# Kernel tuning notes

Hardware: AMD Instinct MI355X
Metric: run time of the kernel (lower is better)

The kernel has to match this reference:

```python
import jax, jax.numpy as jnp
import numpy as np

N = 50000      # nodes
E = 800000     # edges (before self-loops)
IN = 256
HID = 256
OUT = 128
D = 4
K = 4
K1 = 8
NUM_KS = K1 * ((1 << K) - 1)   # 120 centroids
S = HID // D                   # sub-dim per quantization slice
TAU = 1.0


def setup_inputs() -> dict:
    key = jax.random.key(0)
    ks = jax.random.split(key, 9)
    x = jax.random.normal(ks[0], (N, IN), jnp.float32)
    edge_index = jax.random.randint(ks[1], (2, E), 0, N, dtype=jnp.int64)
    def lin(k, fan_in, fan_out):
        return jax.random.normal(k, (fan_in, fan_out), jnp.float32) / np.float32(np.sqrt(fan_in))
    W0 = lin(ks[2], IN, HID); b0 = jnp.zeros((HID,), jnp.float32)
    W1 = lin(ks[3], HID, HID); b1 = jnp.zeros((HID,), jnp.float32)
    W2 = lin(ks[4], HID, OUT); b2 = jnp.zeros((OUT,), jnp.float32)
    # kaiming_normal on (NUM_KS, HID): std = sqrt(2 / fan_in), fan_in = HID
    centroids = jax.random.normal(ks[5], (NUM_KS, HID), jnp.float32) * np.float32(np.sqrt(2.0 / HID))
    return dict(x=x, edge_index=edge_index, W0=W0, b0=b0, W1=W1, b1=b1, W2=W2, b2=b2,
                centroids=centroids)


def gcn_conv(x, W, b, src, dst):
    # PyG GCNConv: add self-loops, symmetric normalization, aggregate at target
    n = x.shape[0]
    loops = jnp.arange(n, dtype=src.dtype)
    s2 = jnp.concatenate([src, loops])
    d2 = jnp.concatenate([dst, loops])
    deg = jax.ops.segment_sum(jnp.ones_like(d2, x.dtype), d2, num_segments=n)
    dinv = jnp.where(deg > 0, jax.lax.rsqrt(deg), 0.0)
    norm = dinv[s2] * dinv[d2]                      # [E+n]
    xw = x @ W                                      # [n, out]
    out = jax.ops.segment_sum(xw[s2] * norm[:, None], d2, num_segments=n)
    return out + b


def quantize(H, C):
    # H: [n, HID], C: [NUM_KS, HID]
    n = H.shape[0]
    Hr = H.reshape(n, D, S)
    Cr = C.reshape(NUM_KS, D, S)
    # products[n,k,d] = sum_s H[n,d,s] * C[k,d,s]
    prods = jnp.einsum('nds,kds->nkd', Hr, Cr) / TAU   # [n, NUM_KS, D]
    soft_l, hard_l, prob_l = [], [], []
    off = 0
    d_idx = jnp.arange(D)[None, :]
    for j in range(K):                 # K fixed small groups of sizes k_1<<j
        m = K1 << j
        sl = prods[:, off:off + m, :]                  # [n, m, D]
        p = jax.nn.softmax(sl, axis=1)                 # scatter_softmax within group
        Cg = Cr[off:off + m]                           # [m, D, S]
        soft_l.append(jnp.einsum('nmd,mds->nds', p, Cg))
        idx = jnp.argmax(sl, axis=1)                   # [n, D] scatter_max within group
        hard_l.append(Cg[idx, d_idx, :])               # [n, D, S]
        prob_l.append(p)
        off += m
    soft = jnp.stack(soft_l, 1).reshape(n, K, HID)
    hard = jnp.stack(hard_l, 1).reshape(n, K, HID)
    q = jax.lax.stop_gradient(hard - soft) + soft      # straight-through
    balance = jnp.concatenate(prob_l, 1).sum(0) / n    # [NUM_KS, D]
    k_blns = jnp.concatenate([jnp.full((K1 << j,), 1.0 / (K1 << j), jnp.float32) for j in range(K)])
    target = jnp.broadcast_to(k_blns[:, None], (NUM_KS, D))
    reg = jnp.linalg.norm(balance - target)
    pred = jnp.max(q, axis=1)                          # [n, HID]
    return pred, reg


def reference(x, edge_index, W0, b0, W1, b1, W2, b2, centroids):
    src, dst = edge_index[0], edge_index[1]
    h = jax.nn.leaky_relu(gcn_conv(x, W0, b0, src, dst), negative_slope=0.5)
    h = jax.nn.leaky_relu(gcn_conv(h, W1, b1, src, dst), negative_slope=0.5)
    pred, reg = quantize(h, centroids)
    h = h + pred
    out = gcn_conv(h, W2, b2, src, dst)
    return out, reg
```

## Files before the change

### kernel.cpp

```cpp
#include <hip/hip_runtime.h>
#include <math.h>


typedef short bf16x8 __attribute__((ext_vector_type(8)));
typedef float f32x4 __attribute__((ext_vector_type(4)));

__device__ __forceinline__ unsigned short bf16_rne(float a) {
    unsigned u = __builtin_bit_cast(unsigned, a);
    return (unsigned short)((u + 0x7FFFu + ((u >> 16) & 1u)) >> 16);
}
__device__ __forceinline__ float bf16_to_f(unsigned short h) {
    return __builtin_bit_cast(float, (unsigned)h << 16);
}
__device__ __forceinline__ void split4(const float* e, unsigned short* h, unsigned short* l) {
#pragma unroll
    for (int t = 0; t < 4; ++t) {
        h[t] = bf16_rne(e[t]);
        l[t] = bf16_rne(e[t] - bf16_to_f(h[t]));
    }
}


__global__ void k_init(int* cnt, int* cursor, int* counter, float* balance, int n) {
    int i = blockIdx.x * blockDim.x + threadIdx.x;
    if (i < n) { cnt[i] = 0; cursor[i] = 0; }
    if (i < 480) balance[i] = 0.f;
    if (i == 0) *counter = 0;
}

__global__ void k_count(const int* __restrict__ dst, int* __restrict__ cnt, int e) {
    int i = blockIdx.x * blockDim.x + threadIdx.x;
    if (i < e) atomicAdd(&cnt[dst[i]], 1);
}

__global__ void k_dinv(const int* __restrict__ cnt, float* __restrict__ dinv, int n) {
    int i = blockIdx.x * blockDim.x + threadIdx.x;
    if (i < n) dinv[i] = rsqrtf((float)cnt[i] + 1.0f);
}

__global__ void k_alloc(const int* __restrict__ cnt, int* __restrict__ row_start,
                        int* __restrict__ counter, int n) {
    int i = blockIdx.x * blockDim.x + threadIdx.x;
    if (i < n) row_start[i] = atomicAdd(counter, cnt[i]);
}

__global__ void k_fill(const int* __restrict__ src, const int* __restrict__ dst,
                       const float* __restrict__ dinv, const int* __restrict__ row_start,
                       int* __restrict__ cursor, int* __restrict__ csr_src,
                       float* __restrict__ csr_norm, int e) {
    int i = blockIdx.x * blockDim.x + threadIdx.x;
    if (i >= e) return;
    int s = src[i], d = dst[i];
    int slot = atomicAdd(&cursor[d], 1);
    int idx = row_start[d] + slot;
    csr_src[idx] = s;
    csr_norm[idx] = dinv[s] * dinv[d];
}


__global__ void k_splitW(const float* __restrict__ W, short* __restrict__ Th,
                         short* __restrict__ Tl, int N) {
    int i = blockIdx.x * blockDim.x + threadIdx.x;
    if (i >= N * 256) return;
    int nn = i >> 8, kk = i & 255;
    float v = W[kk * N + nn];
    unsigned short h = bf16_rne(v);
    unsigned short l = bf16_rne(v - bf16_to_f(h));
    Th[i] = (short)h;
    Tl[i] = (short)l;
}

__global__ void k_splitA(const float* __restrict__ X, short* __restrict__ Hi,
                         short* __restrict__ Lo, int total8) {
    int i = blockIdx.x * blockDim.x + threadIdx.x;
    if (i >= total8) return;
    float4 a = *(const float4*)(X + (size_t)i * 8);
    float4 b = *(const float4*)(X + (size_t)i * 8 + 4);
    float e0[4] = {a.x, a.y, a.z, a.w}, e1[4] = {b.x, b.y, b.z, b.w};
    unsigned short h0[4], l0[4], h1[4], l1[4];
    split4(e0, h0, l0);
    split4(e1, h1, l1);
    *(uint4*)(Hi + (size_t)i * 8) = make_uint4(h0[0] | (h0[1] << 16), h0[2] | (h0[3] << 16),
                                              h1[0] | (h1[1] << 16), h1[2] | (h1[3] << 16));
    *(uint4*)(Lo + (size_t)i * 8) = make_uint4(l0[0] | (l0[1] << 16), l0[2] | (l0[3] << 16),
                                              l1[0] | (l1[1] << 16), l1[2] | (l1[3] << 16));
}


__global__ __launch_bounds__(256, 2) void k_gemm_bf16s(const short* __restrict__ Ah,
                                                       const short* __restrict__ Al,
                                                       const short* __restrict__ Bh,
                                                       const short* __restrict__ Bl,
                                                       float* __restrict__ C,
                                                       int M, int N) {
    __shared__ short smem[4 * 128 * 56];
    short* Ash = smem;
    short* Asl = smem + 7168;
    short* Bsh = smem + 14336;
    short* Bsl = smem + 21504;
    const int tid = threadIdx.x;
    const int bm = blockIdx.x * 128;
    const int bn = blockIdx.y * 128;
    const int wave = tid >> 6, lane = tid & 63;
    const int wr = wave >> 1, wc = wave & 1;
    const int lr = lane & 15, lk = lane >> 4;

    int srow[2], ssg[2];
    bool aval[2];
#pragma unroll
    for (int it = 0; it < 2; ++it) {
        int u = it * 256 + tid;
        srow[it] = u >> 2;
        ssg[it] = (u & 3) << 3;
        aval[it] = (bm + srow[it]) < M;
    }

    const bf16x8 z8 = {0, 0, 0, 0, 0, 0, 0, 0};
    bf16x8 pah[2], pal[2], pbh[2], pbl[2];

    auto prefetch = [&](int k0) {
#pragma unroll
        for (int it = 0; it < 2; ++it) {
            size_t arow = (size_t)(bm + srow[it]) * 256 + k0 + ssg[it];
            size_t brow = (size_t)(bn + srow[it]) * 256 + k0 + ssg[it];
            pah[it] = aval[it] ? *(const bf16x8*)(Ah + arow) : z8;
            pal[it] = aval[it] ? *(const bf16x8*)(Al + arow) : z8;
            pbh[it] = *(const bf16x8*)(Bh + brow);
            pbl[it] = *(const bf16x8*)(Bl + brow);
        }
    };

    f32x4 acc[4][4] = {};
    prefetch(0);

    for (int k0 = 0; k0 < 256; k0 += 32) {
#pragma unroll
        for (int it = 0; it < 2; ++it) {
            int off = srow[it] * 56 + ssg[it];
            *(bf16x8*)&Ash[off] = pah[it];
            *(bf16x8*)&Asl[off] = pal[it];
            *(bf16x8*)&Bsh[off] = pbh[it];
            *(bf16x8*)&Bsl[off] = pbl[it];
        }
        __syncthreads();

        bf16x8 ah[4], al[4], bh[4], bl[4];
#pragma unroll
        for (int i = 0; i < 4; ++i) {
            int off = (wr * 64 + i * 16 + lr) * 56 + lk * 8;
            ah[i] = *(bf16x8*)&Ash[off];
            al[i] = *(bf16x8*)&Asl[off];
        }
#pragma unroll
        for (int j = 0; j < 4; ++j) {
            int off = (wc * 64 + j * 16 + lr) * 56 + lk * 8;
            bh[j] = *(bf16x8*)&Bsh[off];
            bl[j] = *(bf16x8*)&Bsl[off];
        }

        if (k0 < 224) prefetch(k0 + 32);

#pragma unroll
        for (int i = 0; i < 4; ++i)
#pragma unroll
            for (int j = 0; j < 4; ++j) {
                acc[i][j] = __builtin_amdgcn_mfma_f32_16x16x32_bf16(al[i], bh[j], acc[i][j], 0, 0, 0);
                acc[i][j] = __builtin_amdgcn_mfma_f32_16x16x32_bf16(ah[i], bl[j], acc[i][j], 0, 0, 0);
                acc[i][j] = __builtin_amdgcn_mfma_f32_16x16x32_bf16(ah[i], bh[j], acc[i][j], 0, 0, 0);
            }
        __syncthreads();
    }

    float* Cs = (float*)smem;
#pragma unroll
    for (int p = 0; p < 2; ++p) {
        if (wc == p) {
#pragma unroll
            for (int i = 0; i < 4; ++i)
#pragma unroll
                for (int r = 0; r < 4; ++r) {
                    int row = wr * 64 + i * 16 + lk * 4 + r;
#pragma unroll
                    for (int j = 0; j < 4; ++j)
                        Cs[row * 68 + j * 16 + lr] = acc[i][j][r];
                }
        }
        __syncthreads();
#pragma unroll
        for (int t = 0; t < 8; ++t) {
            int idx = t * 256 + tid;
            int row = idx >> 4, c4 = idx & 15;
            if (bm + row < M)
                *(float4*)(C + (size_t)(bm + row) * N + bn + p * 64 + c4 * 4) =
                    *(const float4*)&Cs[row * 68 + c4 * 4];
        }
        __syncthreads();
    }
}


template <bool RELU, int MODE>
__global__ __launch_bounds__(256, 4) void k_agg4(const float* __restrict__ xw,
                                                 const float* __restrict__ dinv,
                                                 const int* __restrict__ csr_src,
                                                 const float* __restrict__ csr_norm,
                                                 const int* __restrict__ row_start,
                                                 const int* __restrict__ cnt,
                                                 const float* __restrict__ bias,
                                                 float* __restrict__ out,
                                                 short* __restrict__ outH,
                                                 short* __restrict__ outL, int n) {
    int node = blockIdx.x * 4 + (threadIdx.x >> 6);
    if (node >= n) return;
    int lane = threadIdx.x & 63;
    int c = lane * 4;
    float di = dinv[node];
    float4 self = *(const float4*)(xw + (size_t)node * 256 + c);
    float4 bv = *(const float4*)(bias + c);
    float sw = di * di;
    float ax = self.x * sw + bv.x;
    float ay = self.y * sw + bv.y;
    float az = self.z * sw + bv.z;
    float aw = self.w * sw + bv.w;
    int st = row_start[node];
    int m = cnt[node];
    for (int t0 = 0; t0 < m; t0 += 64) {
        int rem = m - t0;
        int cnt_i = rem < 64 ? rem : 64;
        int idx_l = 0;
        float nrm_l = 0.f;
        if (lane < cnt_i) {
            idx_l = csr_src[st + t0 + lane];
            nrm_l = csr_norm[st + t0 + lane];
        }
        int t = 0;
        for (; t + 8 <= cnt_i; t += 8) {
            const float* p0 = xw + (size_t)__shfl(idx_l, t + 0, 64) * 256 + c;
            const float* p1 = xw + (size_t)__shfl(idx_l, t + 1, 64) * 256 + c;
            const float* p2 = xw + (size_t)__shfl(idx_l, t + 2, 64) * 256 + c;
            const float* p3 = xw + (size_t)__shfl(idx_l, t + 3, 64) * 256 + c;
            const float* p4 = xw + (size_t)__shfl(idx_l, t + 4, 64) * 256 + c;
            const float* p5 = xw + (size_t)__shfl(idx_l, t + 5, 64) * 256 + c;
            const float* p6 = xw + (size_t)__shfl(idx_l, t + 6, 64) * 256 + c;
            const float* p7 = xw + (size_t)__shfl(idx_l, t + 7, 64) * 256 + c;
            float4 v0 = *(const float4*)p0;
            float4 v1 = *(const float4*)p1;
            float4 v2 = *(const float4*)p2;
            float4 v3 = *(const float4*)p3;
            float4 v4 = *(const float4*)p4;
            float4 v5 = *(const float4*)p5;
            float4 v6 = *(const float4*)p6;
            float4 v7 = *(const float4*)p7;
            float w0 = __shfl(nrm_l, t + 0, 64);
            float w1 = __shfl(nrm_l, t + 1, 64);
            float w2 = __shfl(nrm_l, t + 2, 64);
            float w3 = __shfl(nrm_l, t + 3, 64);
            float w4 = __shfl(nrm_l, t + 4, 64);
            float w5 = __shfl(nrm_l, t + 5, 64);
            float w6 = __shfl(nrm_l, t + 6, 64);
            float w7 = __shfl(nrm_l, t + 7, 64);
            ax += v0.x * w0; ay += v0.y * w0; az += v0.z * w0; aw += v0.w * w0;
            ax += v1.x * w1; ay += v1.y * w1; az += v1.z * w1; aw += v1.w * w1;
            ax += v2.x * w2; ay += v2.y * w2; az += v2.z * w2; aw += v2.w * w2;
            ax += v3.x * w3; ay += v3.y * w3; az += v3.z * w3; aw += v3.w * w3;
            ax += v4.x * w4; ay += v4.y * w4; az += v4.z * w4; aw += v4.w * w4;
            ax += v5.x * w5; ay += v5.y * w5; az += v5.z * w5; aw += v5.w * w5;
            ax += v6.x * w6; ay += v6.y * w6; az += v6.z * w6; aw += v6.w * w6;
            ax += v7.x * w7; ay += v7.y * w7; az += v7.z * w7; aw += v7.w * w7;
        }
        for (; t < cnt_i; ++t) {
            int s = __shfl(idx_l, t, 64);
            float w = __shfl(nrm_l, t, 64);
            float4 v = *(const float4*)(xw + (size_t)s * 256 + c);
            ax += v.x * w; ay += v.y * w; az += v.z * w; aw += v.w * w;
        }
    }
    if (RELU) {
        ax = ax > 0.f ? ax : 0.5f * ax;
        ay = ay > 0.f ? ay : 0.5f * ay;
        az = az > 0.f ? az : 0.5f * az;
        aw = aw > 0.f ? aw : 0.5f * aw;
    }
    if (MODE == 0) {
        *(float4*)(out + (size_t)node * 256 + c) = make_float4(ax, ay, az, aw);
    } else {
        float e[4] = {ax, ay, az, aw};
        unsigned short h[4], l[4];
        split4(e, h, l);
        size_t o = (size_t)node * 256 + c;
        *(uint2*)(outH + o) = make_uint2(h[0] | (h[1] << 16), h[2] | (h[3] << 16));
        *(uint2*)(outL + o) = make_uint2(l[0] | (l[1] << 16), l[2] | (l[3] << 16));
    }
}

__global__ __launch_bounds__(256, 4) void k_agg2(const float* __restrict__ xw,
                                                 const float* __restrict__ dinv,
                                                 const int* __restrict__ csr_src,
                                                 const float* __restrict__ csr_norm,
                                                 const int* __restrict__ row_start,
                                                 const int* __restrict__ cnt,
                                                 const float* __restrict__ bias,
                                                 float* __restrict__ out, int n) {
    int node = blockIdx.x * 4 + (threadIdx.x >> 6);
    if (node >= n) return;
    int lane = threadIdx.x & 63;
    int c = lane * 2;
    float di = dinv[node];
    float2 self = *(const float2*)(xw + (size_t)node * 128 + c);
    float2 bv = *(const float2*)(bias + c);
    float sw = di * di;
    float ax = self.x * sw + bv.x;
    float ay = self.y * sw + bv.y;
    int st = row_start[node];
    int m = cnt[node];
    for (int t0 = 0; t0 < m; t0 += 64) {
        int rem = m - t0;
        int cnt_i = rem < 64 ? rem : 64;
        int idx_l = 0;
        float nrm_l = 0.f;
        if (lane < cnt_i) {
            idx_l = csr_src[st + t0 + lane];
            nrm_l = csr_norm[st + t0 + lane];
        }
        int t = 0;
        for (; t + 8 <= cnt_i; t += 8) {
            const float* p0 = xw + (size_t)__shfl(idx_l, t + 0, 64) * 128 + c;
            const float* p1 = xw + (size_t)__shfl(idx_l, t + 1, 64) * 128 + c;
            const float* p2 = xw + (size_t)__shfl(idx_l, t + 2, 64) * 128 + c;
            const float* p3 = xw + (size_t)__shfl(idx_l, t + 3, 64) * 128 + c;
            const float* p4 = xw + (size_t)__shfl(idx_l, t + 4, 64) * 128 + c;
            const float* p5 = xw + (size_t)__shfl(idx_l, t + 5, 64) * 128 + c;
            const float* p6 = xw + (size_t)__shfl(idx_l, t + 6, 64) * 128 + c;
            const float* p7 = xw + (size_t)__shfl(idx_l, t + 7, 64) * 128 + c;
            float2 v0 = *(const float2*)p0;
            float2 v1 = *(const float2*)p1;
            float2 v2 = *(const float2*)p2;
            float2 v3 = *(const float2*)p3;
            float2 v4 = *(const float2*)p4;
            float2 v5 = *(const float2*)p5;
            float2 v6 = *(const float2*)p6;
            float2 v7 = *(const float2*)p7;
            float w0 = __shfl(nrm_l, t + 0, 64);
            float w1 = __shfl(nrm_l, t + 1, 64);
            float w2 = __shfl(nrm_l, t + 2, 64);
            float w3 = __shfl(nrm_l, t + 3, 64);
            float w4 = __shfl(nrm_l, t + 4, 64);
            float w5 = __shfl(nrm_l, t + 5, 64);
            float w6 = __shfl(nrm_l, t + 6, 64);
            float w7 = __shfl(nrm_l, t + 7, 64);
            ax += v0.x * w0; ay += v0.y * w0;
            ax += v1.x * w1; ay += v1.y * w1;
            ax += v2.x * w2; ay += v2.y * w2;
            ax += v3.x * w3; ay += v3.y * w3;
            ax += v4.x * w4; ay += v4.y * w4;
            ax += v5.x * w5; ay += v5.y * w5;
            ax += v6.x * w6; ay += v6.y * w6;
            ax += v7.x * w7; ay += v7.y * w7;
        }
        for (; t < cnt_i; ++t) {
            int s = __shfl(idx_l, t, 64);
            float w = __shfl(nrm_l, t, 64);
            float2 v = *(const float2*)(xw + (size_t)s * 128 + c);
            ax += v.x * w; ay += v.y * w;
        }
    }
    *(float2*)(out + (size_t)node * 128 + c) = make_float2(ax, ay);
}


__global__ __launch_bounds__(256, 4) void k_quant4(const float* __restrict__ h2,
                                                   const float* __restrict__ cent,
                                                   short* __restrict__ h3h,
                                                   short* __restrict__ h3l,
                                                   float* __restrict__ balance_g, int n) {
    __shared__ float As[32 * 132];
    __shared__ float Bs[32 * 132];
    __shared__ float bal4[4 * 128];
    __shared__ int km_ls[128 * 4];
    const int tid = threadIdx.x;
    const int n0 = blockIdx.x * 128;
    const int d = blockIdx.y;
    const int ty = tid >> 4, tx = tid & 15;
    const int wave = tid >> 6, lane = tid & 63;

    int gid, base, sz;
    if (tx == 0)       { gid = 0; base = 0;  sz = 1; }
    else if (tx <= 2)  { gid = 1; base = 1;  sz = 2; }
    else if (tx <= 6)  { gid = 2; base = 3;  sz = 4; }
    else if (tx <= 14) { gid = 3; base = 7;  sz = 8; }
    else               { gid = 0; base = 15; sz = 0; }
    const int l = tx - base;
    const int segbase = lane & 48;

    {
        int k = tid >> 3, r = tid & 7;
        int col = (r < 4) ? (60 + r) : (120 + r);
        Bs[k * 132 + col] = 0.f;
    }

    const int srow = tid >> 3, sk4 = tid & 7;
    const bool srv = (n0 + srow) < n;
    float acc[8][8] = {};

#pragma unroll
    for (int it = 0; it < 4; ++it) {
        int row = srow + it * 32;
        float4 v = make_float4(0.f, 0.f, 0.f, 0.f);
        if (n0 + row < n)
            v = *(const float4*)(h2 + (size_t)(n0 + row) * 256 + d * 64 + sk4 * 4);
        As[(sk4 * 4 + 0) * 132 + row] = v.x;
        As[(sk4 * 4 + 1) * 132 + row] = v.y;
        As[(sk4 * 4 + 2) * 132 + row] = v.z;
        As[(sk4 * 4 + 3) * 132 + row] = v.w;
    }
#pragma unroll
    for (int it = 0; it < 4; ++it) {
        int q = it * 256 + tid;
        if (q < 960) {
            int cc = q >> 3, k4 = q & 7;
            float4 v = *(const float4*)(cent + (size_t)cc * 256 + d * 64 + k4 * 4);
            int col = ((cc >> 3) << 2) + (((cc >> 2) & 1) << 6) + (cc & 3);
            Bs[(k4 * 4 + 0) * 132 + col] = v.x;
            Bs[(k4 * 4 + 1) * 132 + col] = v.y;
            Bs[(k4 * 4 + 2) * 132 + col] = v.z;
            Bs[(k4 * 4 + 3) * 132 + col] = v.w;
        }
    }
    float4 ph[4];
#pragma unroll
    for (int it = 0; it < 4; ++it) {
        int row = srow + it * 32;
        ph[it] = make_float4(0.f, 0.f, 0.f, 0.f);
        if (n0 + row < n)
            ph[it] = *(const float4*)(h2 + (size_t)(n0 + row) * 256 + d * 64 + 32 + sk4 * 4);
    }
    __syncthreads();

#pragma unroll 4
    for (int k = 0; k < 32; ++k) {
        float4 a0 = *(const float4*)&As[k * 132 + ty * 8];
        float4 a1 = *(const float4*)&As[k * 132 + ty * 8 + 4];
        float4 b0 = *(const float4*)&Bs[k * 132 + tx * 4];
        float4 b1 = *(const float4*)&Bs[k * 132 + 64 + tx * 4];
        float av[8] = {a0.x, a0.y, a0.z, a0.w, a1.x, a1.y, a1.z, a1.w};
        float bv[8] = {b0.x, b0.y, b0.z, b0.w, b1.x, b1.y, b1.z, b1.w};
#pragma unroll
        for (int i = 0; i < 8; ++i)
#pragma unroll
            for (int j = 0; j < 8; ++j)
                acc[i][j] += av[i] * bv[j];
    }
    __syncthreads();

#pragma unroll
    for (int it = 0; it < 4; ++it) {
        int row = srow + it * 32;
        As[(sk4 * 4 + 0) * 132 + row] = ph[it].x;
        As[(sk4 * 4 + 1) * 132 + row] = ph[it].y;
        As[(sk4 * 4 + 2) * 132 + row] = ph[it].z;
        As[(sk4 * 4 + 3) * 132 + row] = ph[it].w;
    }
#pragma unroll
    for (int it = 0; it < 4; ++it) {
        int q = it * 256 + tid;
        if (q < 960) {
            int cc = q >> 3, k4 = q & 7;
            float4 v = *(const float4*)(cent + (size_t)cc * 256 + d * 64 + 32 + k4 * 4);
            int col = ((cc >> 3) << 2) + (((cc >> 2) & 1) << 6) + (cc & 3);
            Bs[(k4 * 4 + 0) * 132 + col] = v.x;
            Bs[(k4 * 4 + 1) * 132 + col] = v.y;
            Bs[(k4 * 4 + 2) * 132 + col] = v.z;
            Bs[(k4 * 4 + 3) * 132 + col] = v.w;
        }
    }
    __syncthreads();

#pragma unroll 4
    for (int k = 0; k < 32; ++k) {
        float4 a0 = *(const float4*)&As[k * 132 + ty * 8];
        float4 a1 = *(const float4*)&As[k * 132 + ty * 8 + 4];
        float4 b0 = *(const float4*)&Bs[k * 132 + tx * 4];
        float4 b1 = *(const float4*)&Bs[k * 132 + 64 + tx * 4];
        float av[8] = {a0.x, a0.y, a0.z, a0.w, a1.x, a1.y, a1.z, a1.w};
        float bv[8] = {b0.x, b0.y, b0.z, b0.w, b1.x, b1.y, b1.z, b1.w};
#pragma unroll
        for (int i = 0; i < 8; ++i)
#pragma unroll
            for (int j = 0; j < 8; ++j)
                acc[i][j] += av[i] * bv[j];
    }

    float balp[8] = {};
#pragma unroll
    for (int i = 0; i < 8; ++i) {
        const int node = ty * 8 + i;
        const bool act = (n0 + node) < n;
        float m = acc[i][0];
        int am = tx * 8;
#pragma unroll
        for (int j = 1; j < 8; ++j)
            if (acc[i][j] > m) { m = acc[i][j]; am = tx * 8 + j; }
#pragma unroll
        for (int s = 1; s <= 4; s <<= 1) {
            int pl = l ^ s;
            int srcl = segbase + base + pl;
            float mo = __shfl(m, srcl, 64);
            int amo = __shfl(am, srcl, 64);
            if (pl < sz && (mo > m || (mo == m && amo < am))) { m = mo; am = amo; }
        }
        float Z = 0.f;
#pragma unroll
        for (int j = 0; j < 8; ++j) {
            float e2 = expf(acc[i][j] - m);
            acc[i][j] = e2;
            Z += e2;
        }
#pragma unroll
        for (int s = 1; s <= 4; s <<= 1) {
            int pl = l ^ s;
            int srcl = segbase + base + pl;
            float Zo = __shfl(Z, srcl, 64);
            if (pl < sz) Z += Zo;
        }
        float invZ = (act && sz > 0) ? (1.0f / Z) : 0.f;
#pragma unroll
        for (int j = 0; j < 8; ++j) balp[j] += acc[i][j] * invZ;
        if (l == 0 && sz > 0) km_ls[node * 4 + gid] = am;
    }

#pragma unroll
    for (int j = 0; j < 8; ++j) {
        float v = balp[j];
        v += __shfl_xor(v, 16, 64);
        v += __shfl_xor(v, 32, 64);
        balp[j] = v;
    }
    if (lane < 16) {
#pragma unroll
        for (int j = 0; j < 8; ++j)
            bal4[wave * 128 + tx * 8 + j] = balp[j];
    }
    __syncthreads();
    if (tid < 120) {
        float s = bal4[tid] + bal4[128 + tid] + bal4[256 + tid] + bal4[384 + tid];
        atomicAdd(&balance_g[tid * 4 + d], s);
    }

    {
        const int node = tid >> 1;
        const int half = tid & 1;
        if (n0 + node < n) {
            int k0 = km_ls[node * 4 + 0], k1 = km_ls[node * 4 + 1];
            int k2 = km_ls[node * 4 + 2], k3 = km_ls[node * 4 + 3];
            const float* hp = h2 + (size_t)(n0 + node) * 256 + d * 64 + half * 32;
            const float* c0 = cent + (size_t)k0 * 256 + d * 64 + half * 32;
            const float* c1 = cent + (size_t)k1 * 256 + d * 64 + half * 32;
            const float* c2 = cent + (size_t)k2 * 256 + d * 64 + half * 32;
            const float* c3 = cent + (size_t)k3 * 256 + d * 64 + half * 32;
            size_t obase = (size_t)(n0 + node) * 256 + d * 64 + half * 32;
#pragma unroll
            for (int q = 0; q < 8; ++q) {
                int g = q * 4;
                float4 hv = *(const float4*)(hp + g);
                float4 v0 = *(const float4*)(c0 + g);
                float4 v1 = *(const float4*)(c1 + g);
                float4 v2 = *(const float4*)(c2 + g);
                float4 v3 = *(const float4*)(c3 + g);
                float e[4];
                e[0] = hv.x + fmaxf(fmaxf(v0.x, v1.x), fmaxf(v2.x, v3.x));
                e[1] = hv.y + fmaxf(fmaxf(v0.y, v1.y), fmaxf(v2.y, v3.y));
                e[2] = hv.z + fmaxf(fmaxf(v0.z, v1.z), fmaxf(v2.z, v3.z));
                e[3] = hv.w + fmaxf(fmaxf(v0.w, v1.w), fmaxf(v2.w, v3.w));
                unsigned short h[4], l[4];
                split4(e, h, l);
                *(uint2*)(h3h + obase + g) = make_uint2(h[0] | (h[1] << 16), h[2] | (h[3] << 16));
                *(uint2*)(h3l + obase + g) = make_uint2(l[0] | (l[1] << 16), l[2] | (l[3] << 16));
            }
        }
    }
}

__global__ void k_reg(const float* __restrict__ balance_g, float* __restrict__ out_reg,
                      float inv_n) {
    __shared__ float red[512];
    int tid = threadIdx.x;
    float v = 0.f;
    if (tid < 480) {
        int k = tid >> 2;
        float target = (k < 8) ? 0.125f : (k < 24) ? 0.0625f : (k < 56) ? 0.03125f : 0.015625f;
        float b = balance_g[tid] * inv_n;
        float df = b - target;
        v = df * df;
    }
    red[tid] = v;
    __syncthreads();
    for (int s = 256; s > 0; s >>= 1) {
        if (tid < s) red[tid] += red[tid + s];
        __syncthreads();
    }
    if (tid == 0) *out_reg = sqrtf(red[0]);
}


extern "C" void kernel_launch(void* const* d_in, const int* in_sizes, int n_in,
                              void* d_out, int out_size, void* d_ws, size_t ws_size,
                              hipStream_t stream) {
    const float* x    = (const float*)d_in[0];
    const int*   ei   = (const int*)d_in[1];
    const float* W0   = (const float*)d_in[2];
    const float* b0   = (const float*)d_in[3];
    const float* W1   = (const float*)d_in[4];
    const float* b1   = (const float*)d_in[5];
    const float* W2   = (const float*)d_in[6];
    const float* b2   = (const float*)d_in[7];
    const float* cent = (const float*)d_in[8];
    const int n = in_sizes[0] / 256;
    const int e = in_sizes[1] / 2;
    const int* src = ei;
    const int* dst = ei + e;
    float* out = (float*)d_out;

    char* w = (char*)d_ws;
    float* bufA = (float*)w;      w += (size_t)n * 256 * 4;
    float* bufB = (float*)w;      w += (size_t)n * 256 * 4;
    float* dinv = (float*)w;      w += (size_t)n * 4;
    int* cnt = (int*)w;           w += (size_t)n * 4;
    int* row_start = (int*)w;     w += (size_t)n * 4;
    int* cursor = (int*)w;        w += (size_t)n * 4;
    int* csr_src = (int*)w;       w += (size_t)e * 4;
    float* csr_norm = (float*)w;  w += (size_t)e * 4;
    int* counter = (int*)w;       w += 256;
    float* balance = (float*)w;   w += 480 * 4;
    short* w0h = (short*)w;       w += 256 * 256 * 2;
    short* w0l = (short*)w;       w += 256 * 256 * 2;
    short* w1h = (short*)w;       w += 256 * 256 * 2;
    short* w1l = (short*)w;       w += 256 * 256 * 2;
    short* w2h = (short*)w;       w += 128 * 256 * 2;
    short* w2l = (short*)w;       w += 128 * 256 * 2;

    short* xh = (short*)bufA;
    short* xl = xh + (size_t)n * 256;
    short* h1h = (short*)bufA;
    short* h1l = h1h + (size_t)n * 256;
    short* h3h = (short*)bufB;
    short* h3l = h3h + (size_t)n * 256;

    const int tb = 256;
    k_init<<<(n + tb - 1) / tb, tb, 0, stream>>>(cnt, cursor, counter, balance, n);
    k_count<<<(e + tb - 1) / tb, tb, 0, stream>>>(dst, cnt, e);
    k_dinv<<<(n + tb - 1) / tb, tb, 0, stream>>>(cnt, dinv, n);
    k_alloc<<<(n + tb - 1) / tb, tb, 0, stream>>>(cnt, row_start, counter, n);
    k_fill<<<(e + tb - 1) / tb, tb, 0, stream>>>(src, dst, dinv, row_start, cursor,
                                                 csr_src, csr_norm, e);

    k_splitW<<<(256 * 256 + tb - 1) / tb, tb, 0, stream>>>(W0, w0h, w0l, 256);
    k_splitW<<<(256 * 256 + tb - 1) / tb, tb, 0, stream>>>(W1, w1h, w1l, 256);
    k_splitW<<<(128 * 256 + tb - 1) / tb, tb, 0, stream>>>(W2, w2h, w2l, 128);
    k_splitA<<<(n * 32 + tb - 1) / tb, tb, 0, stream>>>(x, xh, xl, n * 32);

    dim3 g1((n + 127) / 128, 2);
    k_gemm_bf16s<<<g1, 256, 0, stream>>>(xh, xl, w0h, w0l, bufB, n, 256);
    k_agg4<true, 1><<<(n + 3) / 4, 256, 0, stream>>>(bufB, dinv, csr_src, csr_norm,
                                                     row_start, cnt, b0, nullptr,
                                                     h1h, h1l, n);
    k_gemm_bf16s<<<g1, 256, 0, stream>>>(h1h, h1l, w1h, w1l, bufB, n, 256);
    k_agg4<true, 0><<<(n + 3) / 4, 256, 0, stream>>>(bufB, dinv, csr_src, csr_norm,
                                                     row_start, cnt, b1, bufA,
                                                     nullptr, nullptr, n);

    dim3 gq((n + 127) / 128, 4);
    k_quant4<<<gq, 256, 0, stream>>>(bufA, cent, h3h, h3l, balance, n);

    dim3 g3((n + 127) / 128, 1);
    k_gemm_bf16s<<<g3, 256, 0, stream>>>(h3h, h3l, w2h, w2l, bufA, n, 128);
    k_agg2<<<(n + 3) / 4, 256, 0, stream>>>(bufA, dinv, csr_src, csr_norm,
                                            row_start, cnt, b2, out, n);
    k_reg<<<1, 512, 0, stream>>>(balance, out + (size_t)n * 128, 1.0f / (float)n);
}
```

Baseline: 611.7 us.

## Fold GCN normalization into GEMM epilogue and move quantizer to split-bf16 MFMA

Result: slower. 652.0 us (+6.6%).

```diff
diff --git a/kernel.cpp b/kernel.cpp
--- a/kernel.cpp
+++ b/kernel.cpp
@@ -33,41 +33,49 @@
     if (i < e) atomicAdd(&cnt[dst[i]], 1);
 }
 
-__global__ void k_dinv(const int* __restrict__ cnt, float* __restrict__ dinv, int n) {
+__global__ void k_allocdinv(const int* __restrict__ cnt, int* __restrict__ row_start,
+                            int* __restrict__ counter, float* __restrict__ dinv, int n) {
     int i = blockIdx.x * blockDim.x + threadIdx.x;
-    if (i < n) dinv[i] = rsqrtf((float)cnt[i] + 1.0f);
-}
-
-__global__ void k_alloc(const int* __restrict__ cnt, int* __restrict__ row_start,
-                        int* __restrict__ counter, int n) {
-    int i = blockIdx.x * blockDim.x + threadIdx.x;
-    if (i < n) row_start[i] = atomicAdd(counter, cnt[i]);
+    if (i < n) {
+        row_start[i] = atomicAdd(counter, cnt[i]);
+        dinv[i] = rsqrtf((float)cnt[i] + 1.0f);
+    }
 }
 
 __global__ void k_fill(const int* __restrict__ src, const int* __restrict__ dst,
-                       const float* __restrict__ dinv, const int* __restrict__ row_start,
-                       int* __restrict__ cursor, int* __restrict__ csr_src,
-                       float* __restrict__ csr_norm, int e) {
+                       const int* __restrict__ row_start, int* __restrict__ cursor,
+                       int* __restrict__ csr_src, int e) {
     int i = blockIdx.x * blockDim.x + threadIdx.x;
     if (i >= e) return;
     int s = src[i], d = dst[i];
     int slot = atomicAdd(&cursor[d], 1);
-    int idx = row_start[d] + slot;
-    csr_src[idx] = s;
-    csr_norm[idx] = dinv[s] * dinv[d];
-}
-
-
-__global__ void k_splitW(const float* __restrict__ W, short* __restrict__ Th,
-                         short* __restrict__ Tl, int N) {
+    csr_src[row_start[d] + slot] = s;
+}
+
+
+__global__ void k_splitWC(const float* __restrict__ W0, const float* __restrict__ W1,
+                          const float* __restrict__ W2, const float* __restrict__ cent,
+                          short* __restrict__ w0h, short* __restrict__ w0l,
+                          short* __restrict__ w1h, short* __restrict__ w1l,
+                          short* __restrict__ w2h, short* __restrict__ w2l,
+                          short* __restrict__ ch, short* __restrict__ cl) {
     int i = blockIdx.x * blockDim.x + threadIdx.x;
-    if (i >= N * 256) return;
-    int nn = i >> 8, kk = i & 255;
-    float v = W[kk * N + nn];
+    float v;
+    short *ph, *pl;
+    int j;
+    if (i < 65536) {
+        j = i; v = W0[(j & 255) * 256 + (j >> 8)]; ph = w0h; pl = w0l;
+    } else if (i < 131072) {
+        j = i - 65536; v = W1[(j & 255) * 256 + (j >> 8)]; ph = w1h; pl = w1l;
+    } else if (i < 163840) {
+        j = i - 131072; v = W2[(j & 255) * 128 + (j >> 8)]; ph = w2h; pl = w2l;
+    } else {
+        j = i - 163840; int c = j >> 8;
+        v = (c < 120) ? cent[j] : 0.f; ph = ch; pl = cl;
+    }
     unsigned short h = bf16_rne(v);
-    unsigned short l = bf16_rne(v - bf16_to_f(h));
-    Th[i] = (short)h;
-    Tl[i] = (short)l;
+    ph[j] = (short)h;
+    pl[j] = (short)bf16_rne(v - bf16_to_f(h));
 }
 
 __global__ void k_splitA(const float* __restrict__ X, short* __restrict__ Hi,
@@ -91,6 +99,7 @@
                                                        const short* __restrict__ Al,
                                                        const short* __restrict__ Bh,
                                                        const short* __restrict__ Bl,
+                                                       const float* __restrict__ dinv,
                                                        float* __restrict__ C,
                                                        int M, int N) {
     __shared__ short smem[4 * 128 * 56];
@@ -190,9 +199,12 @@
         for (int t = 0; t < 8; ++t) {
             int idx = t * 256 + tid;
             int row = idx >> 4, c4 = idx & 15;
-            if (bm + row < M)
-                *(float4*)(C + (size_t)(bm + row) * N + bn + p * 64 + c4 * 4) =
-                    *(const float4*)&Cs[row * 68 + c4 * 4];
+            if (bm + row < M) {
+                float s = dinv[bm + row];
+                float4 v = *(const float4*)&Cs[row * 68 + c4 * 4];
+                v.x *= s; v.y *= s; v.z *= s; v.w *= s;
+                *(float4*)(C + (size_t)(bm + row) * N + bn + p * 64 + c4 * 4) = v;
+            }
         }
         __syncthreads();
     }
@@ -203,7 +215,6 @@
 __global__ __launch_bounds__(256, 4) void k_agg4(const float* __restrict__ xw,
                                                  const float* __restrict__ dinv,
                                                  const int* __restrict__ csr_src,
-                                                 const float* __restrict__ csr_norm,
                                                  const int* __restrict__ row_start,
                                                  const int* __restrict__ cnt,
                                                  const float* __restrict__ bias,
@@ -214,25 +225,15 @@
     if (node >= n) return;
     int lane = threadIdx.x & 63;
     int c = lane * 4;
-    float di = dinv[node];
     float4 self = *(const float4*)(xw + (size_t)node * 256 + c);
-    float4 bv = *(const float4*)(bias + c);
-    float sw = di * di;
-    float ax = self.x * sw + bv.x;
-    float ay = self.y * sw + bv.y;
-    float az = self.z * sw + bv.z;
-    float aw = self.w * sw + bv.w;
+    float ax = self.x, ay = self.y, az = self.z, aw = self.w;
     int st = row_start[node];
     int m = cnt[node];
     for (int t0 = 0; t0 < m; t0 += 64) {
         int rem = m - t0;
         int cnt_i = rem < 64 ? rem : 64;
         int idx_l = 0;
-        float nrm_l = 0.f;
-        if (lane < cnt_i) {
-            idx_l = csr_src[st + t0 + lane];
-            nrm_l = csr_norm[st + t0 + lane];
-        }
+        if (lane < cnt_i) idx_l = csr_src[st + t0 + lane];
         int t = 0;
         for (; t + 8 <= cnt_i; t += 8) {
             const float* p0 = xw + (size_t)__shfl(idx_l, t + 0, 64) * 256 + c;
@@ -251,30 +252,27 @@
             float4 v5 = *(const float4*)p5;
             float4 v6 = *(const float4*)p6;
             float4 v7 = *(const float4*)p7;
-            float w0 = __shfl(nrm_l, t + 0, 64);
-            float w1 = __shfl(nrm_l, t + 1, 64);
-            float w2 = __shfl(nrm_l, t + 2, 64);
-            float w3 = __shfl(nrm_l, t + 3, 64);
-            float w4 = __shfl(nrm_l, t + 4, 64);
-            float w5 = __shfl(nrm_l, t + 5, 64);
-            float w6 = __shfl(nrm_l, t + 6, 64);
-            float w7 = __shfl(nrm_l, t + 7, 64);
-            ax += v0.x * w0; ay += v0.y * w0; az += v0.z * w0; aw += v0.w * w0;
-            ax += v1.x * w1; ay += v1.y * w1; az += v1.z * w1; aw += v1.w * w1;
-            ax += v2.x * w2; ay += v2.y * w2; az += v2.z * w2; aw += v2.w * w2;
-            ax += v3.x * w3; ay += v3.y * w3; az += v3.z * w3; aw += v3.w * w3;
-            ax += v4.x * w4; ay += v4.y * w4; az += v4.z * w4; aw += v4.w * w4;
-            ax += v5.x * w5; ay += v5.y * w5; az += v5.z * w5; aw += v5.w * w5;
-            ax += v6.x * w6; ay += v6.y * w6; az += v6.z * w6; aw += v6.w * w6;
-            ax += v7.x * w7; ay += v7.y * w7; az += v7.z * w7; aw += v7.w * w7;
+            ax += v0.x; ay += v0.y; az += v0.z; aw += v0.w;
+            ax += v1.x; ay += v1.y; az += v1.z; aw += v1.w;
+            ax += v2.x; ay += v2.y; az += v2.z; aw += v2.w;
+            ax += v3.x; ay += v3.y; az += v3.z; aw += v3.w;
+            ax += v4.x; ay += v4.y; az += v4.z; aw += v4.w;
+            ax += v5.x; ay += v5.y; az += v5.z; aw += v5.w;
+            ax += v6.x; ay += v6.y; az += v6.z; aw += v6.w;
+            ax += v7.x; ay += v7.y; az += v7.z; aw += v7.w;
         }
         for (; t < cnt_i; ++t) {
             int s = __shfl(idx_l, t, 64);
-            float w = __shfl(nrm_l, t, 64);
             float4 v = *(const float4*)(xw + (size_t)s * 256 + c);
-            ax += v.x * w; ay += v.y * w; az += v.z * w; aw += v.w * w;
-        }
-    }
+            ax += v.x; ay += v.y; az += v.z; aw += v.w;
+        }
+    }
+    float di = dinv[node];
+    float4 bv = *(const float4*)(bias + c);
+    ax = ax * di + bv.x;
+    ay = ay * di + bv.y;
+    az = az * di + bv.z;
+    aw = aw * di + bv.w;
     if (RELU) {
         ax = ax > 0.f ? ax : 0.5f * ax;
         ay = ay > 0.f ? ay : 0.5f * ay;
@@ -296,7 +294,6 @@
 __global__ __launch_bounds__(256, 4) void k_agg2(const float* __restrict__ xw,
                                                  const float* __restrict__ dinv,
                                                  const int* __restrict__ csr_src,
-                                                 const float* __restrict__ csr_norm,
                                                  const int* __restrict__ row_start,
                                                  const int* __restrict__ cnt,
                                                  const float* __restrict__ bias,
@@ -305,23 +302,15 @@
     if (node >= n) return;
     int lane = threadIdx.x & 63;
     int c = lane * 2;
-    float di = dinv[node];
     float2 self = *(const float2*)(xw + (size_t)node * 128 + c);
-    float2 bv = *(const float2*)(bias + c);
-    float sw = di * di;
-    float ax = self.x * sw + bv.x;
-    float ay = self.y * sw + bv.y;
+    float ax = self.x, ay = self.y;
     int st = row_start[node];
     int m = cnt[node];
     for (int t0 = 0; t0 < m; t0 += 64) {
         int rem = m - t0;
         int cnt_i = rem < 64 ? rem : 64;
         int idx_l = 0;
-        float nrm_l = 0.f;
-        if (lane < cnt_i) {
-            idx_l = csr_src[st + t0 + lane];
-            nrm_l = csr_norm[st + t0 + lane];
-        }
+        if (lane < cnt_i) idx_l = csr_src[st + t0 + lane];
         int t = 0;
         for (; t + 8 <= cnt_i; t += 8) {
             const float* p0 = xw + (size_t)__shfl(idx_l, t + 0, 64) * 128 + c;
@@ -340,205 +329,167 @@
             float2 v5 = *(const float2*)p5;
             float2 v6 = *(const float2*)p6;
             float2 v7 = *(const float2*)p7;
-            float w0 = __shfl(nrm_l, t + 0, 64);
-            float w1 = __shfl(nrm_l, t + 1, 64);
-            float w2 = __shfl(nrm_l, t + 2, 64);
-            float w3 = __shfl(nrm_l, t + 3, 64);
-            float w4 = __shfl(nrm_l, t + 4, 64);
-            float w5 = __shfl(nrm_l, t + 5, 64);
-            float w6 = __shfl(nrm_l, t + 6, 64);
-            float w7 = __shfl(nrm_l, t + 7, 64);
-            ax += v0.x * w0; ay += v0.y * w0;
-            ax += v1.x * w1; ay += v1.y * w1;
-            ax += v2.x * w2; ay += v2.y * w2;
-            ax += v3.x * w3; ay += v3.y * w3;
-            ax += v4.x * w4; ay += v4.y * w4;
-            ax += v5.x * w5; ay += v5.y * w5;
-            ax += v6.x * w6; ay += v6.y * w6;
-            ax += v7.x * w7; ay += v7.y * w7;
+            ax += v0.x; ay += v0.y;
+            ax += v1.x; ay += v1.y;
+            ax += v2.x; ay += v2.y;
+            ax += v3.x; ay += v3.y;
+            ax += v4.x; ay += v4.y;
+            ax += v5.x; ay += v5.y;
+            ax += v6.x; ay += v6.y;
+            ax += v7.x; ay += v7.y;
         }
         for (; t < cnt_i; ++t) {
             int s = __shfl(idx_l, t, 64);
-            float w = __shfl(nrm_l, t, 64);
             float2 v = *(const float2*)(xw + (size_t)s * 128 + c);
-            ax += v.x * w; ay += v.y * w;
-        }
-    }
-    *(float2*)(out + (size_t)node * 128 + c) = make_float2(ax, ay);
-}
-
-
-__global__ __launch_bounds__(256, 4) void k_quant4(const float* __restrict__ h2,
+            ax += v.x; ay += v.y;
+        }
+    }
+    float di = dinv[node];
+    float2 bv = *(const float2*)(bias + c);
+    *(float2*)(out + (size_t)node * 128 + c) = make_float2(ax * di + bv.x, ay * di + bv.y);
+}
+
+
+__global__ __launch_bounds__(256, 3) void k_quant6(const short* __restrict__ h2h,
+                                                   const short* __restrict__ h2l,
+                                                   const short* __restrict__ ch,
+                                                   const short* __restrict__ cl,
                                                    const float* __restrict__ cent,
                                                    short* __restrict__ h3h,
                                                    short* __restrict__ h3l,
                                                    float* __restrict__ balance_g, int n) {
-    __shared__ float As[32 * 132];
-    __shared__ float Bs[32 * 132];
+    __shared__ short Ah[128 * 72];
+    __shared__ short Al[128 * 72];
     __shared__ float bal4[4 * 128];
     __shared__ int km_ls[128 * 4];
     const int tid = threadIdx.x;
     const int n0 = blockIdx.x * 128;
     const int d = blockIdx.y;
-    const int ty = tid >> 4, tx = tid & 15;
     const int wave = tid >> 6, lane = tid & 63;
-
-    int gid, base, sz;
-    if (tx == 0)       { gid = 0; base = 0;  sz = 1; }
-    else if (tx <= 2)  { gid = 1; base = 1;  sz = 2; }
-    else if (tx <= 6)  { gid = 2; base = 3;  sz = 4; }
-    else if (tx <= 14) { gid = 3; base = 7;  sz = 8; }
-    else               { gid = 0; base = 15; sz = 0; }
-    const int l = tx - base;
-    const int segbase = lane & 48;
+    const int l = lane & 15, lk = lane >> 4;
+    const int nib = lane & 48;
 
     {
-        int k = tid >> 3, r = tid & 7;
-        int col = (r < 4) ? (60 + r) : (120 + r);
-        Bs[k * 132 + col] = 0.f;
-    }
-
-    const int srow = tid >> 3, sk4 = tid & 7;
-    const bool srv = (n0 + srow) < n;
-    float acc[8][8] = {};
-
-#pragma unroll
-    for (int it = 0; it < 4; ++it) {
-        int row = srow + it * 32;
-        float4 v = make_float4(0.f, 0.f, 0.f, 0.f);
-        if (n0 + row < n)
-            v = *(const float4*)(h2 + (size_t)(n0 + row) * 256 + d * 64 + sk4 * 4);
-        As[(sk4 * 4 + 0) * 132 + row] = v.x;
-        As[(sk4 * 4 + 1) * 132 + row] = v.y;
-        As[(sk4 * 4 + 2) * 132 + row] = v.z;
-        As[(sk4 * 4 + 3) * 132 + row] = v.w;
-    }
-#pragma unroll
-    for (int it = 0; it < 4; ++it) {
-        int q = it * 256 + tid;
-        if (q < 960) {
-            int cc = q >> 3, k4 = q & 7;
-            float4 v = *(const float4*)(cent + (size_t)cc * 256 + d * 64 + k4 * 4);
-            int col = ((cc >> 3) << 2) + (((cc >> 2) & 1) << 6) + (cc & 3);
-            Bs[(k4 * 4 + 0) * 132 + col] = v.x;
-            Bs[(k4 * 4 + 1) * 132 + col] = v.y;
-            Bs[(k4 * 4 + 2) * 132 + col] = v.z;
-            Bs[(k4 * 4 + 3) * 132 + col] = v.w;
-        }
-    }
-    float4 ph[4];
-#pragma unroll
-    for (int it = 0; it < 4; ++it) {
-        int row = srow + it * 32;
-        ph[it] = make_float4(0.f, 0.f, 0.f, 0.f);
-        if (n0 + row < n)
-            ph[it] = *(const float4*)(h2 + (size_t)(n0 + row) * 256 + d * 64 + 32 + sk4 * 4);
+        const int row = tid >> 1, half = tid & 1;
+        const size_t g = (size_t)(n0 + row) * 256 + d * 64 + half * 32;
+        const int o = row * 72 + half * 32;
+        const bf16x8 z8 = {0, 0, 0, 0, 0, 0, 0, 0};
+        bool v = (n0 + row) < n;
+#pragma unroll
+        for (int s = 0; s < 4; ++s) {
+            *(bf16x8*)&Ah[o + s * 8] = v ? *(const bf16x8*)(h2h + g + s * 8) : z8;
+            *(bf16x8*)&Al[o + s * 8] = v ? *(const bf16x8*)(h2l + g + s * 8) : z8;
+        }
     }
     __syncthreads();
 
-#pragma unroll 4
-    for (int k = 0; k < 32; ++k) {
-        float4 a0 = *(const float4*)&As[k * 132 + ty * 8];
-        float4 a1 = *(const float4*)&As[k * 132 + ty * 8 + 4];
-        float4 b0 = *(const float4*)&Bs[k * 132 + tx * 4];
-        float4 b1 = *(const float4*)&Bs[k * 132 + 64 + tx * 4];
-        float av[8] = {a0.x, a0.y, a0.z, a0.w, a1.x, a1.y, a1.z, a1.w};
-        float bv[8] = {b0.x, b0.y, b0.z, b0.w, b1.x, b1.y, b1.z, b1.w};
-#pragma unroll
-        for (int i = 0; i < 8; ++i)
-#pragma unroll
-            for (int j = 0; j < 8; ++j)
-                acc[i][j] += av[i] * bv[j];
-    }
-    __syncthreads();
-
-#pragma unroll
-    for (int it = 0; it < 4; ++it) {
-        int row = srow + it * 32;
-        As[(sk4 * 4 + 0) * 132 + row] = ph[it].x;
-        As[(sk4 * 4 + 1) * 132 + row] = ph[it].y;
-        As[(sk4 * 4 + 2) * 132 + row] = ph[it].z;
-        As[(sk4 * 4 + 3) * 132 + row] = ph[it].w;
-    }
-#pragma unroll
-    for (int it = 0; it < 4; ++it) {
-        int q = it * 256 + tid;
-        if (q < 960) {
-            int cc = q >> 3, k4 = q & 7;
-            float4 v = *(const float4*)(cent + (size_t)cc * 256 + d * 64 + 32 + k4 * 4);
-            int col = ((cc >> 3) << 2) + (((cc >> 2) & 1) << 6) + (cc & 3);
-            Bs[(k4 * 4 + 0) * 132 + col] = v.x;
-            Bs[(k4 * 4 + 1) * 132 + col] = v.y;
-            Bs[(k4 * 4 + 2) * 132 + col] = v.z;
-            Bs[(k4 * 4 + 3) * 132 + col] = v.w;
-        }
-    }
-    __syncthreads();
-
-#pragma unroll 4
-    for (int k = 0; k < 32; ++k) {
-        float4 a0 = *(const float4*)&As[k * 132 + ty * 8];
-        float4 a1 = *(const float4*)&As[k * 132 + ty * 8 + 4];
-        float4 b0 = *(const float4*)&Bs[k * 132 + tx * 4];
-        float4 b1 = *(const float4*)&Bs[k * 132 + 64 + tx * 4];
-        float av[8] = {a0.x, a0.y, a0.z, a0.w, a1.x, a1.y, a1.z, a1.w};
-        float bv[8] = {b0.x, b0.y, b0.z, b0.w, b1.x, b1.y, b1.z, b1.w};
-#pragma unroll
-        for (int i = 0; i < 8; ++i)
-#pragma unroll
-            for (int j = 0; j < 8; ++j)
-                acc[i][j] += av[i] * bv[j];
-    }
+    f32x4 acc[2][8] = {};
+#pragma unroll
+    for (int kc = 0; kc < 2; ++kc) {
+        bf16x8 ah[2], al[2];
+#pragma unroll
+        for (int t = 0; t < 2; ++t) {
+            int off = (wave * 32 + t * 16 + l) * 72 + kc * 32 + lk * 8;
+            ah[t] = *(const bf16x8*)&Ah[off];
+            al[t] = *(const bf16x8*)&Al[off];
+        }
+#pragma unroll
+        for (int ct = 0; ct < 8; ++ct) {
+            size_t boff = (size_t)(ct * 16 + l) * 256 + d * 64 + kc * 32 + lk * 8;
+            bf16x8 bh = *(const bf16x8*)(ch + boff);
+            bf16x8 bl = *(const bf16x8*)(cl + boff);
+#pragma unroll
+            for (int t = 0; t < 2; ++t) {
+                acc[t][ct] = __builtin_amdgcn_mfma_f32_16x16x32_bf16(al[t], bh, acc[t][ct], 0, 0, 0);
+                acc[t][ct] = __builtin_amdgcn_mfma_f32_16x16x32_bf16(ah[t], bl, acc[t][ct], 0, 0, 0);
+                acc[t][ct] = __builtin_amdgcn_mfma_f32_16x16x32_bf16(ah[t], bh, acc[t][ct], 0, 0, 0);
+            }
+        }
+    }
+
+    int gof[8];
+    gof[0] = (l < 8) ? 0 : 1;
+    gof[1] = (l < 8) ? 1 : 2;
+    gof[2] = 2;
+    gof[3] = (l < 8) ? 2 : 3;
+    gof[4] = 3; gof[5] = 3; gof[6] = 3;
+    gof[7] = (l < 8) ? 3 : -1;
 
     float balp[8] = {};
-#pragma unroll
-    for (int i = 0; i < 8; ++i) {
-        const int node = ty * 8 + i;
-        const bool act = (n0 + node) < n;
-        float m = acc[i][0];
-        int am = tx * 8;
-#pragma unroll
-        for (int j = 1; j < 8; ++j)
-            if (acc[i][j] > m) { m = acc[i][j]; am = tx * 8 + j; }
-#pragma unroll
-        for (int s = 1; s <= 4; s <<= 1) {
-            int pl = l ^ s;
-            int srcl = segbase + base + pl;
-            float mo = __shfl(m, srcl, 64);
-            int amo = __shfl(am, srcl, 64);
-            if (pl < sz && (mo > m || (mo == m && amo < am))) { m = mo; am = amo; }
-        }
-        float Z = 0.f;
-#pragma unroll
-        for (int j = 0; j < 8; ++j) {
-            float e2 = expf(acc[i][j] - m);
-            acc[i][j] = e2;
-            Z += e2;
-        }
-#pragma unroll
-        for (int s = 1; s <= 4; s <<= 1) {
-            int pl = l ^ s;
-            int srcl = segbase + base + pl;
-            float Zo = __shfl(Z, srcl, 64);
-            if (pl < sz) Z += Zo;
-        }
-        float invZ = (act && sz > 0) ? (1.0f / Z) : 0.f;
-#pragma unroll
-        for (int j = 0; j < 8; ++j) balp[j] += acc[i][j] * invZ;
-        if (l == 0 && sz > 0) km_ls[node * 4 + gid] = am;
-    }
-
-#pragma unroll
-    for (int j = 0; j < 8; ++j) {
-        float v = balp[j];
-        v += __shfl_xor(v, 16, 64);
-        v += __shfl_xor(v, 32, 64);
-        balp[j] = v;
+
+#pragma unroll
+    for (int t = 0; t < 2; ++t)
+#pragma unroll
+        for (int r = 0; r < 4; ++r) {
+            const int node = wave * 32 + t * 16 + lk * 4 + r;
+            const bool act = (n0 + node) < n;
+            float v[8];
+#pragma unroll
+            for (int ct = 0; ct < 8; ++ct) v[ct] = acc[t][ct][r];
+
+            float mg[4];
+            int ag[4];
+#pragma unroll
+            for (int g = 0; g < 4; ++g) {
+                float m = -3.4e38f;
+                int am = 0x7FFFFFFF;
+#pragma unroll
+                for (int ct = 0; ct < 8; ++ct)
+                    if (gof[ct] == g && v[ct] > m) { m = v[ct]; am = ct * 16 + l; }
+#pragma unroll
+                for (int s = 1; s <= 8; s <<= 1) {
+                    int srcl = nib | (l ^ s);
+                    float mo = __shfl(m, srcl, 64);
+                    int amo = __shfl(am, srcl, 64);
+                    if (mo > m || (mo == m && amo < am)) { m = mo; am = amo; }
+                }
+                mg[g] = m;
+                ag[g] = am;
+            }
+            float e[8];
+            float Z[4] = {0.f, 0.f, 0.f, 0.f};
+#pragma unroll
+            for (int ct = 0; ct < 8; ++ct) {
+                float ms = (gof[ct] == 0) ? mg[0] : (gof[ct] == 1) ? mg[1]
+                         : (gof[ct] == 2) ? mg[2] : mg[3];
+                e[ct] = (gof[ct] >= 0) ? expf(v[ct] - ms) : 0.f;
+            }
+#pragma unroll
+            for (int g = 0; g < 4; ++g) {
+#pragma unroll
+                for (int ct = 0; ct < 8; ++ct)
+                    if (gof[ct] == g) Z[g] += e[ct];
+#pragma unroll
+                for (int s = 1; s <= 8; s <<= 1) {
+                    int srcl = nib | (l ^ s);
+                    Z[g] += __shfl(Z[g], srcl, 64);
+                }
+            }
+            float iz[4];
+#pragma unroll
+            for (int g = 0; g < 4; ++g) iz[g] = act ? (1.0f / Z[g]) : 0.f;
+#pragma unroll
+            for (int ct = 0; ct < 8; ++ct) {
+                float s = (gof[ct] == 0) ? iz[0] : (gof[ct] == 1) ? iz[1]
+                        : (gof[ct] == 2) ? iz[2] : (gof[ct] == 3) ? iz[3] : 0.f;
+                balp[ct] += e[ct] * s;
+            }
+            if (l == 0) {
+#pragma unroll
+                for (int g = 0; g < 4; ++g) km_ls[node * 4 + g] = ag[g];
+            }
+        }
+
+#pragma unroll
+    for (int ct = 0; ct < 8; ++ct) {
+        float b = balp[ct];
+        b += __shfl_xor(b, 16, 64);
+        b += __shfl_xor(b, 32, 64);
+        balp[ct] = b;
     }
     if (lane < 16) {
 #pragma unroll
-        for (int j = 0; j < 8; ++j)
-            bal4[wave * 128 + tx * 8 + j] = balp[j];
+        for (int ct = 0; ct < 8; ++ct) bal4[wave * 128 + ct * 16 + l] = balp[ct];
     }
     __syncthreads();
     if (tid < 120) {
@@ -552,29 +503,32 @@
         if (n0 + node < n) {
             int k0 = km_ls[node * 4 + 0], k1 = km_ls[node * 4 + 1];
             int k2 = km_ls[node * 4 + 2], k3 = km_ls[node * 4 + 3];
-            const float* hp = h2 + (size_t)(n0 + node) * 256 + d * 64 + half * 32;
             const float* c0 = cent + (size_t)k0 * 256 + d * 64 + half * 32;
             const float* c1 = cent + (size_t)k1 * 256 + d * 64 + half * 32;
             const float* c2 = cent + (size_t)k2 * 256 + d * 64 + half * 32;
             const float* c3 = cent + (size_t)k3 * 256 + d * 64 + half * 32;
+            const int ao = node * 72 + half * 32;
             size_t obase = (size_t)(n0 + node) * 256 + d * 64 + half * 32;
 #pragma unroll
             for (int q = 0; q < 8; ++q) {
                 int g = q * 4;
-                float4 hv = *(const float4*)(hp + g);
                 float4 v0 = *(const float4*)(c0 + g);
                 float4 v1 = *(const float4*)(c1 + g);
                 float4 v2 = *(const float4*)(c2 + g);
                 float4 v3 = *(const float4*)(c3 + g);
                 float e[4];
-                e[0] = hv.x + fmaxf(fmaxf(v0.x, v1.x), fmaxf(v2.x, v3.x));
-                e[1] = hv.y + fmaxf(fmaxf(v0.y, v1.y), fmaxf(v2.y, v3.y));
-                e[2] = hv.z + fmaxf(fmaxf(v0.z, v1.z), fmaxf(v2.z, v3.z));
-                e[3] = hv.w + fmaxf(fmaxf(v0.w, v1.w), fmaxf(v2.w, v3.w));
-                unsigned short h[4], l[4];
-                split4(e, h, l);
+#pragma unroll
+                for (int u = 0; u < 4; ++u) {
+                    float hv = bf16_to_f((unsigned short)Ah[ao + g + u]) +
+                               bf16_to_f((unsigned short)Al[ao + g + u]);
+                    float m0 = fmaxf(fmaxf(((const float*)&v0)[u], ((const float*)&v1)[u]),
+                                     fmaxf(((const float*)&v2)[u], ((const float*)&v3)[u]));
+                    e[u] = hv + m0;
+                }
+                unsigned short h[4], lo[4];
+                split4(e, h, lo);
                 *(uint2*)(h3h + obase + g) = make_uint2(h[0] | (h[1] << 16), h[2] | (h[3] << 16));
-                *(uint2*)(h3l + obase + g) = make_uint2(l[0] | (l[1] << 16), l[2] | (l[3] << 16));
+                *(uint2*)(h3l + obase + g) = make_uint2(lo[0] | (lo[1] << 16), lo[2] | (lo[3] << 16));
             }
         }
     }
@@ -628,7 +582,6 @@
     int* row_start = (int*)w;     w += (size_t)n * 4;
     int* cursor = (int*)w;        w += (size_t)n * 4;
     int* csr_src = (int*)w;       w += (size_t)e * 4;
-    float* csr_norm = (float*)w;  w += (size_t)e * 4;
     int* counter = (int*)w;       w += 256;
     float* balance = (float*)w;   w += 480 * 4;
     short* w0h = (short*)w;       w += 256 * 256 * 2;
@@ -637,43 +590,42 @@
     short* w1l = (short*)w;       w += 256 * 256 * 2;
     short* w2h = (short*)w;       w += 128 * 256 * 2;
     short* w2l = (short*)w;       w += 128 * 256 * 2;
+    short* ch  = (short*)w;       w += 128 * 256 * 2;
+    short* cl  = (short*)w;       w += 128 * 256 * 2;
 
     short* xh = (short*)bufA;
     short* xl = xh + (size_t)n * 256;
     short* h1h = (short*)bufA;
     short* h1l = h1h + (size_t)n * 256;
+    short* h2h = (short*)bufA;
+    short* h2l = h2h + (size_t)n * 256;
     short* h3h = (short*)bufB;
     short* h3l = h3h + (size_t)n * 256;
 
     const int tb = 256;
     k_init<<<(n + tb - 1) / tb, tb, 0, stream>>>(cnt, cursor, counter, balance, n);
     k_count<<<(e + tb - 1) / tb, tb, 0, stream>>>(dst, cnt, e);
-    k_dinv<<<(n + tb - 1) / tb, tb, 0, stream>>>(cnt, dinv, n);
-    k_alloc<<<(n + tb - 1) / tb, tb, 0, stream>>>(cnt, row_start, counter, n);
-    k_fill<<<(e + tb - 1) / tb, tb, 0, stream>>>(src, dst, dinv, row_start, cursor,
-                                                 csr_src, csr_norm, e);
-
-    k_splitW<<<(256 * 256 + tb - 1) / tb, tb, 0, stream>>>(W0, w0h, w0l, 256);
-    k_splitW<<<(256 * 256 + tb - 1) / tb, tb, 0, stream>>>(W1, w1h, w1l, 256);
-    k_splitW<<<(128 * 256 + tb - 1) / tb, tb, 0, stream>>>(W2, w2h, w2l, 128);
+    k_allocdinv<<<(n + tb - 1) / tb, tb, 0, stream>>>(cnt, row_start, counter, dinv, n);
+    k_fill<<<(e + tb - 1) / tb, tb, 0, stream>>>(src, dst, row_start, cursor, csr_src, e);
+
+    k_splitWC<<<196608 / tb, tb, 0, stream>>>(W0, W1, W2, cent, w0h, w0l, w1h, w1l,
+                                              w2h, w2l, ch, cl);
     k_splitA<<<(n * 32 + tb - 1) / tb, tb, 0, stream>>>(x, xh, xl, n * 32);
 
     dim3 g1((n + 127) / 128, 2);
-    k_gemm_bf16s<<<g1, 256, 0, stream>>>(xh, xl, w0h, w0l, bufB, n, 256);
-    k_agg4<true, 1><<<(n + 3) / 4, 256, 0, stream>>>(bufB, dinv, csr_src, csr_norm,
-                                                     row_start, cnt, b0, nullptr,
-                                                     h1h, h1l, n);
-    k_gemm_bf16s<<<g1, 256, 0, stream>>>(h1h, h1l, w1h, w1l, bufB, n, 256);
-    k_agg4<true, 0><<<(n + 3) / 4, 256, 0, stream>>>(bufB, dinv, csr_src, csr_norm,
-                                                     row_start, cnt, b1, bufA,
-                                                     nullptr, nullptr, n);
+    k_gemm_bf16s<<<g1, 256, 0, stream>>>(xh, xl, w0h, w0l, dinv, bufB, n, 256);
+    k_agg4<true, 1><<<(n + 3) / 4, 256, 0, stream>>>(bufB, dinv, csr_src, row_start,
+                                                     cnt, b0, nullptr, h1h, h1l, n);
+    k_gemm_bf16s<<<g1, 256, 0, stream>>>(h1h, h1l, w1h, w1l, dinv, bufB, n, 256);
+    k_agg4<true, 1><<<(n + 3) / 4, 256, 0, stream>>>(bufB, dinv, csr_src, row_start,
+                                                     cnt, b1, nullptr, h2h, h2l, n);
 
     dim3 gq((n + 127) / 128, 4);
-    k_quant4<<<gq, 256, 0, stream>>>(bufA, cent, h3h, h3l, balance, n);
+    k_quant6<<<gq, 256, 0, stream>>>(h2h, h2l, ch, cl, cent, h3h, h3l, balance, n);
 
     dim3 g3((n + 127) / 128, 1);
-    k_gemm_bf16s<<<g3, 256, 0, stream>>>(h3h, h3l, w2h, w2l, bufA, n, 128);
-    k_agg2<<<(n + 3) / 4, 256, 0, stream>>>(bufA, dinv, csr_src, csr_norm,
-                                            row_start, cnt, b2, out, n);
+    k_gemm_bf16s<<<g3, 256, 0, stream>>>(h3h, h3l, w2h, w2l, dinv, bufA, n, 128);
+    k_agg2<<<(n + 3) / 4, 256, 0, stream>>>(bufA, dinv, csr_src, row_start,
+                                            cnt, b2, out, n);
     k_reg<<<1, 512, 0, stream>>>(balance, out + (size_t)n * 128, 1.0f / (float)n);
 }
```
